# Kernel tuning notes

Hardware: AMD Instinct MI355X
Metric: run time of the kernel (lower is better)

Reference implementation:

```python
import jax, jax.numpy as jnp
import numpy as np

N, K = 16384, 32          # num bboxes, context size
IN_F, HID = 608, 384      # in_features, hidden_dim
ALPHA = 0.2               # LeakyReLU slope
NEG_INF = -9e15


def setup_inputs() -> dict:
    key = jax.random.key(0)
    k1, k2, k3, k4, k5, k6, k7, k8 = jax.random.split(key, 8)
    h_i = jax.random.normal(k1, (N, IN_F), dtype=jnp.float32)
    idx = jax.random.randint(k2, (N, K), 0, N)
    pad = jax.random.uniform(k3, (N, K)) < 0.2
    context_indices = jnp.where(pad, -1, idx).astype(jnp.int64)
    s_in = 1.0 / np.sqrt(IN_F)
    s_a = 1.0 / np.sqrt(2 * HID)
    W_i = jax.random.uniform(k4, (IN_F, HID), minval=-s_in, maxval=s_in, dtype=jnp.float32)
    W_j = jax.random.uniform(k5, (IN_F, HID), minval=-s_in, maxval=s_in, dtype=jnp.float32)
    a_i = jax.random.uniform(k6, (HID,), minval=-s_a, maxval=s_a, dtype=jnp.float32)
    a_j = jax.random.uniform(k7, (HID,), minval=-s_a, maxval=s_a, dtype=jnp.float32)
    a_b = jax.random.uniform(k8, (1,), minval=-s_a, maxval=s_a, dtype=jnp.float32)
    return {"h_i": h_i, "context_indices": context_indices,
            "W_i": W_i, "W_j": W_j, "a_i": a_i, "a_j": a_j, "a_b": a_b}


def reference(h_i, context_indices, W_i, W_j, a_i, a_j, a_b):
    n = h_i.shape[0]
    Wh_i = h_i @ W_i                          # [N, H]
    # W_j has no bias, so projecting then gathering (zero pad row) equals
    # gathering zero-padded features then projecting.
    Wh_all = h_i @ W_j                        # [N, H]
    Wh_pad = jnp.concatenate([Wh_all, jnp.zeros((1, HID), Wh_all.dtype)], axis=0)
    idx = jnp.where(context_indices >= 0, context_indices, n)   # -1 -> zero row
    Wh_j = Wh_pad[idx]                        # [N, K, H] gather
    # attention_layer(concat(Wh_i, Wh_j)) == Wh_i@a_i + Wh_j@a_j + b
    scores = (Wh_i @ a_i)[:, None] + Wh_j @ a_j + a_b[0]        # [N, K]
    scores = jnp.where(scores > 0, scores, ALPHA * scores)      # LeakyReLU
    scores = jnp.where(context_indices >= 0, scores, NEG_INF)   # mask padding
    att = jax.nn.softmax(scores, axis=1)                        # [N, K]
    h_prime = jnp.einsum('nk,nkh->nh', att, Wh_j)               # [N, H]
    return h_prime
```

## Files before the change

### kernel.cpp

```cpp
#include <hip/hip_runtime.h>
#include <hip/hip_bf16.h>

typedef unsigned short u16;
typedef unsigned int u32;
typedef __attribute__((ext_vector_type(8))) __bf16 bf16x8;
typedef __attribute__((ext_vector_type(4))) float f32x4;

#define KCTX 32
#define INF_ 608
#define HID_ 384

#define HB_OFF  0
#define WH_OFF  19922944
#define BT_OFF  32505856
#define V_OFF   32972800
#define SI_OFF  32975232
#define SJ_OFF  33040768
#define AJF_OFF 33106304
#define ABF_OFF 33107840

__device__ __forceinline__ float bfu(u16 u)  { return __uint_as_float(((u32)u) << 16); }
__device__ __forceinline__ float bflo(u32 u) { return __uint_as_float(u << 16); }
__device__ __forceinline__ float bfhi(u32 u) { return __uint_as_float(u & 0xffff0000u); }
__device__ __forceinline__ u16 f2bf(float x) {
  u32 u = __float_as_uint(x);
  return (u16)((u + 0x7fffu + ((u >> 16) & 1u)) >> 16);
}
__device__ __forceinline__ void async_ld16(const void* g, void* l) {
  __builtin_amdgcn_global_load_lds(
      (const __attribute__((address_space(1))) u32*)g,
      (__attribute__((address_space(3))) u32*)l, 16, 0, 0);
}

__device__ __forceinline__ int detect_f32(const u32* hw) {
  const u32 w = hw[threadIdx.x & 63];
  const int e = (int)((w >> 7) & 0xffu);
  const unsigned long long mb = __ballot(e > 134 || e < 100);
  return __popcll(mb) >= 16;
}
__device__ __forceinline__ int detect_i64(const int* ci) {
  const int hi = ci[2 * (threadIdx.x & 63) + 1];
  const unsigned long long mz = __ballot(hi == 0 || hi == -1);
  return __popcll(mz) >= 48;
}

__global__ __launch_bounds__(256) void prep_kernel(
    const void* __restrict__ h, const void* __restrict__ Wi,
    const void* __restrict__ Wj, const void* __restrict__ ai,
    const void* __restrict__ aj, const void* __restrict__ ab,
    u16* __restrict__ Bt, float* __restrict__ v, float* __restrict__ sj,
    float* __restrict__ ajf, float* __restrict__ abf) {
  __shared__ u16 tile[64][65];
  const int f32m = detect_f32((const u32*)h);
  const int bid = blockIdx.x, tid = threadIdx.x;
  if (bid < 60) {
    const int ft = bid / 6, ht = bid - ft * 6;
    const int f0 = ft * 64, h0 = ht * 64;
    const int ln = tid & 63, fg = tid >> 6;
#pragma unroll
    for (int rr = 0; rr < 16; ++rr) {
      const int fl = fg * 16 + rr;
      const int f = f0 + fl;
      if (f < INF_)
        tile[fl][ln] = f32m ? f2bf(((const float*)Wj)[(size_t)f * HID_ + h0 + ln])
                            : ((const u16*)Wj)[(size_t)f * HID_ + h0 + ln];
    }
    __syncthreads();
#pragma unroll
    for (int rr = 0; rr < 16; ++rr) {
      const int hl = fg * 16 + rr;
      const int f = f0 + ln;
      if (f < INF_) Bt[(size_t)(h0 + hl) * INF_ + f] = tile[ln][hl];
    }
  } else if (bid < 98) {
    const int t = (bid - 60) * 16 + (tid >> 4);
    const int sl = tid & 15;
    if (t < INF_) {
      float s = 0.f;
      if (f32m) {
        const float4* wi = (const float4*)((const float*)Wi + (size_t)t * HID_);
        const float4* a4 = (const float4*)ai;
        for (int c = sl; c < 96; c += 16) {
          float4 x = wi[c], y = a4[c];
          s += x.x * y.x + x.y * y.y + x.z * y.z + x.w * y.w;
        }
      } else {
        const uint4* wi = (const uint4*)((const u16*)Wi + (size_t)t * HID_);
        const uint4* a4 = (const uint4*)ai;
        for (int c = sl; c < 48; c += 16) {
          uint4 x = wi[c], y = a4[c];
          s += bflo(x.x) * bflo(y.x) + bfhi(x.x) * bfhi(y.x)
             + bflo(x.y) * bflo(y.y) + bfhi(x.y) * bfhi(y.y)
             + bflo(x.z) * bflo(y.z) + bfhi(x.z) * bfhi(y.z)
             + bflo(x.w) * bflo(y.w) + bfhi(x.w) * bfhi(y.w);
        }
      }
      s += __shfl_xor(s, 1); s += __shfl_xor(s, 2);
      s += __shfl_xor(s, 4); s += __shfl_xor(s, 8);
      if (sl == 0) v[t] = s;
    }
  } else {
#pragma unroll 8
    for (int j = 0; j < 64; ++j) sj[j * 256 + tid] = 0.f;
    for (int j = tid; j < HID_; j += 256)
      ajf[j] = f32m ? ((const float*)aj)[j] : bfu(((const u16*)aj)[j]);
    if (tid == 0)
      abf[0] = f32m ? ((const float*)ab)[0] : bfu(((const u16*)ab)[0]);
  }
}

__global__ __launch_bounds__(256) void conv_kernel(
    const void* __restrict__ h, const float* __restrict__ v,
    u16* __restrict__ hb, float* __restrict__ si) {
  const int f32m = detect_f32((const u32*)h);
  const int wv = threadIdx.x >> 6, lane = threadIdx.x & 63;
  const int n = blockIdx.x * 4 + wv;
  uint4* hbrow = (uint4*)(hb + (size_t)n * INF_);
  const float4* v4 = (const float4*)v;
  float sum = 0.f;
  if (f32m) {
    const float4* hr = (const float4*)((const float*)h + (size_t)n * INF_);
    for (int c = lane; c < 76; c += 64) {
      float4 x0 = hr[2 * c], x1 = hr[2 * c + 1];
      uint4 o;
      o.x = (u32)f2bf(x0.x) | ((u32)f2bf(x0.y) << 16);
      o.y = (u32)f2bf(x0.z) | ((u32)f2bf(x0.w) << 16);
      o.z = (u32)f2bf(x1.x) | ((u32)f2bf(x1.y) << 16);
      o.w = (u32)f2bf(x1.z) | ((u32)f2bf(x1.w) << 16);
      hbrow[c] = o;
      float4 w0 = v4[2 * c], w1 = v4[2 * c + 1];
      sum += x0.x * w0.x + x0.y * w0.y + x0.z * w0.z + x0.w * w0.w
           + x1.x * w1.x + x1.y * w1.y + x1.z * w1.z + x1.w * w1.w;
    }
  } else {
    const uint4* hr = (const uint4*)((const u16*)h + (size_t)n * INF_);
    for (int c = lane; c < 76; c += 64) {
      uint4 x = hr[c];
      hbrow[c] = x;
      float4 w0 = v4[2 * c], w1 = v4[2 * c + 1];
      sum += bflo(x.x) * w0.x + bfhi(x.x) * w0.y + bflo(x.y) * w0.z + bfhi(x.y) * w0.w
           + bflo(x.z) * w1.x + bfhi(x.z) * w1.y + bflo(x.w) * w1.z + bfhi(x.w) * w1.w;
    }
  }
#pragma unroll
  for (int o = 32; o; o >>= 1) sum += __shfl_xor(sum, o);
  if (lane == 0) si[n] = sum;
}

__global__ __launch_bounds__(256, 2) void gemm_kernel(
    const u16* __restrict__ A, const u16* __restrict__ Bt,
    u16* __restrict__ C, const float* __restrict__ ajf, float* __restrict__ sj) {
  __shared__ __align__(16) u16 As[128][32];
  __shared__ __align__(16) u16 Bs[128][32];
  const int tid  = threadIdx.x;
  const int lane = tid & 63;
  const int wave = tid >> 6;
  const int row0 = blockIdx.x * 128;
  const int col0 = blockIdx.y * 128;
  const int wm = (wave & 1) * 64;
  const int wn = (wave >> 1) * 64;

  f32x4 acc[4][4];
#pragma unroll
  for (int i = 0; i < 4; ++i)
#pragma unroll
    for (int j = 0; j < 4; ++j) acc[i][j] = (f32x4){0.f, 0.f, 0.f, 0.f};

  const int c0 = tid, c1 = tid + 256;
  const int rA0 = c0 >> 2, kc0 = (c0 & 3) * 16;
  const int rA1 = c1 >> 2, kc1 = (c1 & 3) * 16;
  const char* Ab  = (const char*)A;
  const char* Btb = (const char*)Bt;

  for (int kt = 0; kt < 19; ++kt) {
    const size_t kb = (size_t)kt * 64;
    async_ld16(Ab  + (size_t)(row0 + rA0) * 1216 + kb + kc0, (char*)As + c0 * 16);
    async_ld16(Ab  + (size_t)(row0 + rA1) * 1216 + kb + kc1, (char*)As + c1 * 16);
    async_ld16(Btb + (size_t)(col0 + rA0) * 1216 + kb + kc0, (char*)Bs + c0 * 16);
    async_ld16(Btb + (size_t)(col0 + rA1) * 1216 + kb + kc1, (char*)Bs + c1 * 16);
    __syncthreads();

    const int kk = (lane >> 4) * 8;
    const int lm0 = lane & 15;
    bf16x8 af[4], bfr[4];
#pragma unroll
    for (int i = 0; i < 4; ++i) af[i]  = *(const bf16x8*)&As[wm + i * 16 + lm0][kk];
#pragma unroll
    for (int i = 0; i < 4; ++i) bfr[i] = *(const bf16x8*)&Bs[wn + i * 16 + lm0][kk];
#pragma unroll
    for (int im = 0; im < 4; ++im)
#pragma unroll
      for (int in = 0; in < 4; ++in)
        acc[im][in] = __builtin_amdgcn_mfma_f32_16x16x32_bf16(
            af[im], bfr[in], acc[im][in], 0, 0, 0);
    __syncthreads();
  }

  const int lm = lane & 15, lq = lane >> 4;
#pragma unroll
  for (int im = 0; im < 4; ++im)
#pragma unroll
    for (int in = 0; in < 4; ++in) {
      const int colg = col0 + wn + in * 16 + lm;
#pragma unroll
      for (int r = 0; r < 4; ++r) {
        const int rowg = row0 + wm + im * 16 + lq * 4 + r;
        C[(size_t)rowg * HID_ + colg] = f2bf(acc[im][in][r]);
      }
    }
  float ajv[4];
#pragma unroll
  for (int in = 0; in < 4; ++in) ajv[in] = ajf[col0 + wn + in * 16 + lm];
#pragma unroll
  for (int im = 0; im < 4; ++im)
#pragma unroll
    for (int r = 0; r < 4; ++r) {
      float p = acc[im][0][r] * ajv[0] + acc[im][1][r] * ajv[1]
              + acc[im][2][r] * ajv[2] + acc[im][3][r] * ajv[3];
      p += __shfl_xor(p, 1); p += __shfl_xor(p, 2);
      p += __shfl_xor(p, 4); p += __shfl_xor(p, 8);
      if (lm == 0) atomicAdd(&sj[row0 + wm + im * 16 + lq * 4 + r], p);
    }
}

__global__ __launch_bounds__(256) void attn_kernel(
    const void* __restrict__ h, const int* __restrict__ ci,
    const float* __restrict__ si, const float* __restrict__ sj,
    const float* __restrict__ abf, const u16* __restrict__ Wh,
    void* __restrict__ out) {
  const int f32m = detect_f32((const u32*)h);
  const int i64  = detect_i64(ci);
  const int wv = threadIdx.x >> 6, lane = threadIdx.x & 63;
  const int n = blockIdx.x * 4 + wv;

  float att = 0.f; int idxv = 0;
  if (lane < 32) {
    const size_t t = (size_t)n * KCTX + lane;
    int idx;
    if (i64) { int lo = ci[2 * t], hi = ci[2 * t + 1]; idx = (hi < 0) ? -1 : lo; }
    else     { idx = ci[t]; }
    const bool valid = idx >= 0;
    const float sjv = valid ? sj[idx] : 0.f;
    float raw = si[n] + sjv + abf[0];
    float lr = raw > 0.f ? raw : 0.2f * raw;
    float s = valid ? lr : -9e15f;
    float m = s;
#pragma unroll
    for (int o = 16; o; o >>= 1) m = fmaxf(m, __shfl_xor(m, o, 32));
    float p = __expf(s - m);
    float d = p;
#pragma unroll
    for (int o = 16; o; o >>= 1) d += __shfl_xor(d, o, 32);
    att = valid ? p / d : 0.f;
    idxv = valid ? idx : 0;
  }

  if (lane < 48) {
    float a0 = 0, a1 = 0, a2 = 0, a3 = 0, a4 = 0, a5 = 0, a6 = 0, a7 = 0;
#pragma unroll
    for (int kb = 0; kb < KCTX; kb += 8) {
      uint4 q[8]; float ww[8];
#pragma unroll
      for (int u = 0; u < 8; ++u) {
        ww[u] = __shfl(att, kb + u);
        const int j = __shfl(idxv, kb + u);
        q[u] = ((const uint4*)(Wh + (u32)j * HID_))[lane];
      }
#pragma unroll
      for (int u = 0; u < 8; ++u) {
        const float w = ww[u];
        a0 += w * bflo(q[u].x); a1 += w * bfhi(q[u].x);
        a2 += w * bflo(q[u].y); a3 += w * bfhi(q[u].y);
        a4 += w * bflo(q[u].z); a5 += w * bfhi(q[u].z);
        a6 += w * bflo(q[u].w); a7 += w * bfhi(q[u].w);
      }
    }
    if (f32m) {
      float4* o4 = (float4*)out + (size_t)n * 96 + lane * 2;
      o4[0] = (float4){a0, a1, a2, a3};
      o4[1] = (float4){a4, a5, a6, a7};
    } else {
      uint4 o;
      o.x = (u32)f2bf(a0) | ((u32)f2bf(a1) << 16);
      o.y = (u32)f2bf(a2) | ((u32)f2bf(a3) << 16);
      o.z = (u32)f2bf(a4) | ((u32)f2bf(a5) << 16);
      o.w = (u32)f2bf(a6) | ((u32)f2bf(a7) << 16);
      ((uint4*)out)[(size_t)n * 48 + lane] = o;
    }
  }
}

extern "C" void kernel_launch(void* const* d_in, const int* in_sizes, int n_in,
                              void* d_out, int out_size, void* d_ws, size_t ws_size,
                              hipStream_t stream) {
  const void* h  = d_in[0];
  const int*  ci = (const int*)d_in[1];
  const void* Wi = d_in[2];
  const void* Wj = d_in[3];
  const void* ai = d_in[4];
  const void* aj = d_in[5];
  const void* ab = d_in[6];

  char* ws = (char*)d_ws;
  u16*   hb  = (u16*)(ws + HB_OFF);
  u16*   Wh  = (u16*)(ws + WH_OFF);
  u16*   Bt  = (u16*)(ws + BT_OFF);
  float* v   = (float*)(ws + V_OFF);
  float* si  = (float*)(ws + SI_OFF);
  float* sj  = (float*)(ws + SJ_OFF);
  float* ajf = (float*)(ws + AJF_OFF);
  float* abf = (float*)(ws + ABF_OFF);

  prep_kernel<<<99, 256, 0, stream>>>(h, Wi, Wj, ai, aj, ab, Bt, v, sj, ajf, abf);
  conv_kernel<<<4096, 256, 0, stream>>>(h, v, hb, si);
  dim3 g(128, 3);
  gemm_kernel<<<g, 256, 0, stream>>>(hb, Bt, Wh, ajf, sj);
  attn_kernel<<<4096, 256, 0, stream>>>(h, ci, si, sj, abf, Wh, d_out);
}
```

Measured before the change: 160.6 us.

## Fuse bf16 conversion and si dot-product into GEMM with full-row A tiles

Removes the separate conversion kernel and the bf16 copy of h in workspace. Each GEMM block now loads a 32-row strip of h, converts it into a full-K LDS tile, computes si on the fly, and computes all 384 output columns, streaming B tiles from Bt per K step. This saves a full read/write pass of h and a launch, but the grid drops to 512 blocks with large LDS use (about 63 KB), and each row block rereads all of Bt.

```diff
diff --git a/kernel.cpp b/kernel.cpp
--- a/kernel.cpp
+++ b/kernel.cpp
@@ -4,13 +4,13 @@
 typedef unsigned short u16;
 typedef unsigned int u32;
 typedef __attribute__((ext_vector_type(8))) __bf16 bf16x8;
+typedef __attribute__((ext_vector_type(4))) __bf16 bf16x4;
 typedef __attribute__((ext_vector_type(4))) float f32x4;
 
 #define KCTX 32
 #define INF_ 608
 #define HID_ 384
 
-#define HB_OFF  0
 #define WH_OFF  19922944
 #define BT_OFF  32505856
 #define V_OFF   32972800
@@ -109,117 +109,125 @@
   }
 }
 
-__global__ __launch_bounds__(256) void conv_kernel(
-    const void* __restrict__ h, const float* __restrict__ v,
-    u16* __restrict__ hb, float* __restrict__ si) {
-  const int f32m = detect_f32((const u32*)h);
-  const int wv = threadIdx.x >> 6, lane = threadIdx.x & 63;
-  const int n = blockIdx.x * 4 + wv;
-  uint4* hbrow = (uint4*)(hb + (size_t)n * INF_);
-  const float4* v4 = (const float4*)v;
-  float sum = 0.f;
-  if (f32m) {
-    const float4* hr = (const float4*)((const float*)h + (size_t)n * INF_);
-    for (int c = lane; c < 76; c += 64) {
-      float4 x0 = hr[2 * c], x1 = hr[2 * c + 1];
-      uint4 o;
-      o.x = (u32)f2bf(x0.x) | ((u32)f2bf(x0.y) << 16);
-      o.y = (u32)f2bf(x0.z) | ((u32)f2bf(x0.w) << 16);
-      o.z = (u32)f2bf(x1.x) | ((u32)f2bf(x1.y) << 16);
-      o.w = (u32)f2bf(x1.z) | ((u32)f2bf(x1.w) << 16);
-      hbrow[c] = o;
-      float4 w0 = v4[2 * c], w1 = v4[2 * c + 1];
-      sum += x0.x * w0.x + x0.y * w0.y + x0.z * w0.z + x0.w * w0.w
-           + x1.x * w1.x + x1.y * w1.y + x1.z * w1.z + x1.w * w1.w;
-    }
-  } else {
-    const uint4* hr = (const uint4*)((const u16*)h + (size_t)n * INF_);
-    for (int c = lane; c < 76; c += 64) {
-      uint4 x = hr[c];
-      hbrow[c] = x;
-      float4 w0 = v4[2 * c], w1 = v4[2 * c + 1];
-      sum += bflo(x.x) * w0.x + bfhi(x.x) * w0.y + bflo(x.y) * w0.z + bfhi(x.y) * w0.w
-           + bflo(x.z) * w1.x + bfhi(x.z) * w1.y + bflo(x.w) * w1.z + bfhi(x.w) * w1.w;
-    }
-  }
-#pragma unroll
-  for (int o = 32; o; o >>= 1) sum += __shfl_xor(sum, o);
-  if (lane == 0) si[n] = sum;
-}
-
-__global__ __launch_bounds__(256, 2) void gemm_kernel(
-    const u16* __restrict__ A, const u16* __restrict__ Bt,
-    u16* __restrict__ C, const float* __restrict__ ajf, float* __restrict__ sj) {
-  __shared__ __align__(16) u16 As[128][32];
-  __shared__ __align__(16) u16 Bs[128][32];
+__global__ __launch_bounds__(256) void gemm_fused(
+    const void* __restrict__ A,
+    const u16* __restrict__ Bt,
+    const float* __restrict__ v,
+    u16* __restrict__ C,
+    float* __restrict__ si, const float* __restrict__ ajf,
+    float* __restrict__ sj) {
+  __shared__ __align__(16) u16 As[32][612];
+  __shared__ __align__(16) u16 Bs[12288];
+  const int f32m = detect_f32((const u32*)A);
   const int tid  = threadIdx.x;
   const int lane = tid & 63;
-  const int wave = tid >> 6;
-  const int row0 = blockIdx.x * 128;
-  const int col0 = blockIdx.y * 128;
-  const int wm = (wave & 1) * 64;
-  const int wn = (wave >> 1) * 64;
-
-  f32x4 acc[4][4];
-#pragma unroll
-  for (int i = 0; i < 4; ++i)
-#pragma unroll
-    for (int j = 0; j < 4; ++j) acc[i][j] = (f32x4){0.f, 0.f, 0.f, 0.f};
-
-  const int c0 = tid, c1 = tid + 256;
-  const int rA0 = c0 >> 2, kc0 = (c0 & 3) * 16;
-  const int rA1 = c1 >> 2, kc1 = (c1 & 3) * 16;
-  const char* Ab  = (const char*)A;
+  const int wv   = tid >> 6;
+  const int row0 = blockIdx.x * 32;
   const char* Btb = (const char*)Bt;
 
+#pragma unroll
+  for (int i = 0; i < 6; ++i) {
+    const int c = tid + i * 256;
+    async_ld16(Btb + (size_t)(c >> 2) * 1216 + (c & 3) * 16, (char*)Bs + c * 16);
+  }
+
+  {
+    const int g = tid >> 3, sub = tid & 7;
+    float s = 0.f;
+    const float4* v4 = (const float4*)v;
+    if (f32m) {
+      const float4* hr = (const float4*)((const float*)A + (size_t)(row0 + g) * INF_);
+#pragma unroll
+      for (int k = 0; k < 19; ++k) {
+        const int c4 = sub + 8 * k;
+        float4 x = hr[c4];
+        ushort4 sv;
+        sv.x = f2bf(x.x); sv.y = f2bf(x.y); sv.z = f2bf(x.z); sv.w = f2bf(x.w);
+        *(ushort4*)&As[g][c4 * 4] = sv;
+        float4 w = v4[c4];
+        s += x.x * w.x + x.y * w.y + x.z * w.z + x.w * w.w;
+      }
+    } else {
+      const uint4* hr = (const uint4*)((const u16*)A + (size_t)(row0 + g) * INF_);
+      for (int k = 0; k < 10; ++k) {
+        const int c8 = sub + 8 * k;
+        if (c8 < 76) {
+          uint4 x = hr[c8];
+          *(ushort4*)&As[g][c8 * 8]     = *(ushort4*)&x.x;
+          *(ushort4*)&As[g][c8 * 8 + 4] = *(ushort4*)&x.z;
+          float4 w0 = v4[2 * c8], w1 = v4[2 * c8 + 1];
+          s += bflo(x.x) * w0.x + bfhi(x.x) * w0.y + bflo(x.y) * w0.z + bfhi(x.y) * w0.w
+             + bflo(x.z) * w1.x + bfhi(x.z) * w1.y + bflo(x.w) * w1.z + bfhi(x.w) * w1.w;
+        }
+      }
+    }
+    s += __shfl_xor(s, 1); s += __shfl_xor(s, 2); s += __shfl_xor(s, 4);
+    if (sub == 0) si[row0 + g] = s;
+  }
+
+  f32x4 acc[2][6];
+#pragma unroll
+  for (int i = 0; i < 2; ++i)
+#pragma unroll
+    for (int j = 0; j < 6; ++j) acc[i][j] = (f32x4){0.f, 0.f, 0.f, 0.f};
+
+  const int lm = lane & 15, q = lane >> 4;
+  const int n0 = wv * 96;
+
   for (int kt = 0; kt < 19; ++kt) {
-    const size_t kb = (size_t)kt * 64;
-    async_ld16(Ab  + (size_t)(row0 + rA0) * 1216 + kb + kc0, (char*)As + c0 * 16);
-    async_ld16(Ab  + (size_t)(row0 + rA1) * 1216 + kb + kc1, (char*)As + c1 * 16);
-    async_ld16(Btb + (size_t)(col0 + rA0) * 1216 + kb + kc0, (char*)Bs + c0 * 16);
-    async_ld16(Btb + (size_t)(col0 + rA1) * 1216 + kb + kc1, (char*)Bs + c1 * 16);
     __syncthreads();
-
-    const int kk = (lane >> 4) * 8;
-    const int lm0 = lane & 15;
-    bf16x8 af[4], bfr[4];
-#pragma unroll
-    for (int i = 0; i < 4; ++i) af[i]  = *(const bf16x8*)&As[wm + i * 16 + lm0][kk];
-#pragma unroll
-    for (int i = 0; i < 4; ++i) bfr[i] = *(const bf16x8*)&Bs[wn + i * 16 + lm0][kk];
-#pragma unroll
-    for (int im = 0; im < 4; ++im)
-#pragma unroll
-      for (int in = 0; in < 4; ++in)
+    bf16x8 af[2], bfr[6];
+#pragma unroll
+    for (int im = 0; im < 2; ++im) {
+      const int r = im * 16 + lm;
+      bf16x4 lo = *(const bf16x4*)&As[r][kt * 32 + q * 8];
+      bf16x4 hi = *(const bf16x4*)&As[r][kt * 32 + q * 8 + 4];
+      af[im] = __builtin_shufflevector(lo, hi, 0, 1, 2, 3, 4, 5, 6, 7);
+    }
+#pragma unroll
+    for (int in = 0; in < 6; ++in)
+      bfr[in] = *(const bf16x8*)&Bs[(n0 + in * 16 + lm) * 32 + q * 8];
+#pragma unroll
+    for (int im = 0; im < 2; ++im)
+#pragma unroll
+      for (int in = 0; in < 6; ++in)
         acc[im][in] = __builtin_amdgcn_mfma_f32_16x16x32_bf16(
             af[im], bfr[in], acc[im][in], 0, 0, 0);
     __syncthreads();
-  }
-
-  const int lm = lane & 15, lq = lane >> 4;
-#pragma unroll
-  for (int im = 0; im < 4; ++im)
-#pragma unroll
-    for (int in = 0; in < 4; ++in) {
-      const int colg = col0 + wn + in * 16 + lm;
+    if (kt < 18) {
+      const size_t kb = (size_t)(kt + 1) * 64;
+#pragma unroll
+      for (int i = 0; i < 6; ++i) {
+        const int c = tid + i * 256;
+        async_ld16(Btb + (size_t)(c >> 2) * 1216 + kb + (c & 3) * 16, (char*)Bs + c * 16);
+      }
+    }
+  }
+
+#pragma unroll
+  for (int im = 0; im < 2; ++im)
+#pragma unroll
+    for (int in = 0; in < 6; ++in) {
+      const int colg = n0 + in * 16 + lm;
 #pragma unroll
       for (int r = 0; r < 4; ++r) {
-        const int rowg = row0 + wm + im * 16 + lq * 4 + r;
+        const int rowg = row0 + im * 16 + q * 4 + r;
         C[(size_t)rowg * HID_ + colg] = f2bf(acc[im][in][r]);
       }
     }
-  float ajv[4];
-#pragma unroll
-  for (int in = 0; in < 4; ++in) ajv[in] = ajf[col0 + wn + in * 16 + lm];
-#pragma unroll
-  for (int im = 0; im < 4; ++im)
+  float ajv[6];
+#pragma unroll
+  for (int in = 0; in < 6; ++in) ajv[in] = ajf[n0 + in * 16 + lm];
+#pragma unroll
+  for (int im = 0; im < 2; ++im)
 #pragma unroll
     for (int r = 0; r < 4; ++r) {
       float p = acc[im][0][r] * ajv[0] + acc[im][1][r] * ajv[1]
-              + acc[im][2][r] * ajv[2] + acc[im][3][r] * ajv[3];
+              + acc[im][2][r] * ajv[2] + acc[im][3][r] * ajv[3]
+              + acc[im][4][r] * ajv[4] + acc[im][5][r] * ajv[5];
       p += __shfl_xor(p, 1); p += __shfl_xor(p, 2);
       p += __shfl_xor(p, 4); p += __shfl_xor(p, 8);
-      if (lm == 0) atomicAdd(&sj[row0 + wm + im * 16 + lq * 4 + r], p);
+      if (lm == 0) atomicAdd(&sj[row0 + im * 16 + q * 4 + r], p);
     }
 }
 
@@ -302,7 +310,6 @@
   const void* ab = d_in[6];
 
   char* ws = (char*)d_ws;
-  u16*   hb  = (u16*)(ws + HB_OFF);
   u16*   Wh  = (u16*)(ws + WH_OFF);
   u16*   Bt  = (u16*)(ws + BT_OFF);
   float* v   = (float*)(ws + V_OFF);
@@ -312,8 +319,6 @@
   float* abf = (float*)(ws + ABF_OFF);
 
   prep_kernel<<<99, 256, 0, stream>>>(h, Wi, Wj, ai, aj, ab, Bt, v, sj, ajf, abf);
-  conv_kernel<<<4096, 256, 0, stream>>>(h, v, hb, si);
-  dim3 g(128, 3);
-  gemm_kernel<<<g, 256, 0, stream>>>(hb, Bt, Wh, ajf, sj);
+  gemm_fused<<<512, 256, 0, stream>>>(h, Bt, v, Wh, si, ajf, sj);
   attn_kernel<<<4096, 256, 0, stream>>>(h, ci, si, sj, abf, Wh, d_out);
 }
```

Result: faster. 156.7 us (-2.4%).
